# Performance work log

Hardware: AMD Instinct MI355X
Metric: run time of the kernel (lower is better)

The kernel has to match this reference:

```python
import jax, jax.numpy as jnp
import numpy as np

N = 50000
D = 128
E = 600000
R = 8


def setup_inputs() -> dict:
    key = jax.random.key(0)
    ks = jax.random.split(key, 8)
    x = jax.random.normal(ks[0], (N, D), dtype=jnp.float32)
    edge_index = jax.random.randint(ks[1], (2, E), 0, N, dtype=jnp.int64)
    edge_type = jax.random.randint(ks[2], (E,), 0, R, dtype=jnp.int64)
    scale = 1.0 / np.sqrt(D)
    w1 = jax.random.normal(ks[3], (R, D, D), dtype=jnp.float32) * scale
    root1 = jax.random.normal(ks[4], (D, D), dtype=jnp.float32) * scale
    b1 = jnp.zeros((D,), dtype=jnp.float32)
    w2 = jax.random.normal(ks[5], (R, D, D), dtype=jnp.float32) * scale
    root2 = jax.random.normal(ks[6], (D, D), dtype=jnp.float32) * scale
    b2 = jnp.zeros((D,), dtype=jnp.float32)
    return {"x": x, "edge_index": edge_index, "edge_type": edge_type,
            "w1": w1, "root1": root1, "b1": b1,
            "w2": w2, "root2": root2, "b2": b2}


def _rgcn_conv(x, edge_index, edge_type, w, root, b):
    # PyG RGCNConv: per-relation MEAN aggregation of source features over
    # incoming edges, then relation-specific linear, summed over relations,
    # plus root transform and bias.
    src, dst = edge_index[0], edge_index[1]
    # combined segment id: (dst_node, relation) -> one segment_sum pass
    seg = dst * R + edge_type  # [E]
    msgs = x[src]              # [E, D] gather
    sums = jax.ops.segment_sum(msgs, seg, num_segments=N * R).reshape(N, R, D)
    cnts = jax.ops.segment_sum(jnp.ones((msgs.shape[0],), dtype=x.dtype), seg,
                               num_segments=N * R).reshape(N, R, 1)
    mean = sums / jnp.maximum(cnts, 1.0)  # [N, R, D]; empty -> 0
    out = jnp.einsum('nrd,rde->ne', mean, w) + x @ root + b
    return out


def reference(x, edge_index, edge_type, w1, root1, b1, w2, root2, b2):
    # dropout is identity in eval mode
    h = jax.nn.relu(_rgcn_conv(x, edge_index, edge_type, w1, root1, b1))
    out = jax.nn.relu(_rgcn_conv(h, edge_index, edge_type, w2, root2, b2))
    return out
```

## Files before the change

kernel.cpp:

```cpp
#include <hip/hip_runtime.h>

#define NN 50000
#define D 128
#define EE 600000
#define R 8
#define NR (NN * R)
#define SCAN_CHUNK 1024
#define NSB ((NR + SCAN_CHUNK - 1) / SCAN_CHUNK)
#define KO 1152

typedef unsigned short u16;
typedef unsigned int u32;
typedef __attribute__((ext_vector_type(8))) short bf16x8;
typedef __attribute__((ext_vector_type(4))) float f32x4;

__device__ inline u16 f2bf(float f) {
    union { float f; u32 u; } v; v.f = f;
    return (u16)((v.u + 0x7FFFu + ((v.u >> 16) & 1u)) >> 16);
}
__device__ inline float bf2f(u16 h) {
    union { u32 u; float f; } v; v.u = ((u32)h) << 16;
    return v.f;
}

__global__ __launch_bounds__(256) void xcast_kernel(const float2* __restrict__ x2,
                                                    u32* __restrict__ xb, int n) {
    int i = blockIdx.x * 256 + threadIdx.x;
    if (i < n) {
        float2 v = x2[i];
        xb[i] = (u32)f2bf(v.x) | ((u32)f2bf(v.y) << 16);
    }
}

__global__ __launch_bounds__(256) void hist_kernel(const int* __restrict__ dst,
                                                   const int* __restrict__ et,
                                                   int* __restrict__ cnt, int E) {
    int e = blockIdx.x * 256 + threadIdx.x;
    if (e < E) atomicAdd(&cnt[dst[e] * R + et[e]], 1);
}

__global__ __launch_bounds__(256) void scanA(const int* __restrict__ cnt,
                                             int* __restrict__ off,
                                             int* __restrict__ bsum) {
    __shared__ int ts[256];
    const int b = blockIdx.x, t = threadIdx.x;
    const int base = b * SCAN_CHUNK + t * 4;
    int v0 = 0, v1 = 0, v2 = 0, v3 = 0;
    if (base + 3 < NR) {
        int4 q = *(const int4*)(cnt + base);
        v0 = q.x; v1 = q.y; v2 = q.z; v3 = q.w;
    } else {
        if (base < NR) v0 = cnt[base];
        if (base + 1 < NR) v1 = cnt[base + 1];
        if (base + 2 < NR) v2 = cnt[base + 2];
    }
    const int s = v0 + v1 + v2 + v3;
    ts[t] = s;
    __syncthreads();
    for (int d = 1; d < 256; d <<= 1) {
        int x = (t >= d) ? ts[t - d] : 0;
        __syncthreads();
        ts[t] += x;
        __syncthreads();
    }
    const int excl = ts[t] - s;
    if (base < NR) off[base] = excl;
    if (base + 1 < NR) off[base + 1] = excl + v0;
    if (base + 2 < NR) off[base + 2] = excl + v0 + v1;
    if (base + 3 < NR) off[base + 3] = excl + v0 + v1 + v2;
    if (t == 255) bsum[b] = ts[255];
}

__global__ __launch_bounds__(512) void scanB(const int* __restrict__ bsum,
                                             int* __restrict__ boff) {
    __shared__ int ts[512];
    const int t = threadIdx.x;
    const int v = (t < NSB) ? bsum[t] : 0;
    ts[t] = v;
    __syncthreads();
    for (int d = 1; d < 512; d <<= 1) {
        int x = (t >= d) ? ts[t - d] : 0;
        __syncthreads();
        ts[t] += x;
        __syncthreads();
    }
    if (t < NSB) boff[t] = ts[t] - v;
}

__global__ __launch_bounds__(256) void scanC(int* __restrict__ off,
                                             int* __restrict__ cursor,
                                             const int* __restrict__ boff) {
    const int b = blockIdx.x, t = threadIdx.x;
    const int add = boff[b];
    const int base = b * SCAN_CHUNK + t * 4;
#pragma unroll
    for (int j = 0; j < 4; ++j)
        if (base + j < NR) {
            int v = off[base + j] + add;
            off[base + j] = v;
            cursor[base + j] = v;
        }
    if (b == 0 && t == 0) off[NR] = EE;
}

__global__ __launch_bounds__(256) void place_kernel(const int* __restrict__ src,
                                                    const int* __restrict__ dst,
                                                    const int* __restrict__ et,
                                                    const int* __restrict__ cnt,
                                                    int* __restrict__ cursor,
                                                    uint2* __restrict__ edat, int E) {
    int e = blockIdx.x * 256 + threadIdx.x;
    if (e < E) {
        int r = et[e];
        int key = dst[e] * R + r;
        int p = atomicAdd(&cursor[key], 1);
        float s = 1.0f / (float)cnt[key];
        edat[p] = make_uint2((u32)src[e] * (KO / 2) + (u32)r * (D / 2),
                             __float_as_uint(s));
    }
}

__global__ __launch_bounds__(256) void bprep2_kernel(const float* __restrict__ w1,
                                                     const float* __restrict__ root1,
                                                     u16* __restrict__ Bf1,
                                                     const float* __restrict__ w2,
                                                     const float* __restrict__ root2,
                                                     u16* __restrict__ Bf2) {
    int gidx = blockIdx.x * 256 + threadIdx.x;
    if (gidx >= 2 * 9 * 4 * 8 * 64) return;
    const int layer = gidx / (9 * 4 * 8 * 64);
    const int idx = gidx - layer * (9 * 4 * 8 * 64);
    const float* w = layer ? w2 : w1;
    const float* root = layer ? root2 : root1;
    u16* Bfrag = layer ? Bf2 : Bf1;
    const int lane = idx & 63;
    const int g = (idx >> 6) & 7;
    const int kc = (idx >> 9) & 3;
    const int ct = idx >> 11;
    const int col = ct * 128 + g * 16 + (lane & 15);
    const int kbase = kc * 32 + (lane >> 4) * 8;
    u16* o = Bfrag + (size_t)idx * 8;
#pragma unroll
    for (int j = 0; j < 8; ++j) {
        const int k = kbase + j;
        float v = (col < R * D) ? w[(size_t)(col >> 7) * (D * D) + (size_t)k * D + (col & 127)]
                                : root[(size_t)k * D + (col - R * D)];
        o[j] = f2bf(v);
    }
}

__global__ __launch_bounds__(256, 4) void gemm_xw(const u16* __restrict__ xin,
                                                  const u16* __restrict__ Bfrag,
                                                  u16* __restrict__ y) {
    __shared__ uint4 Bs[2048];

    const int t = threadIdx.x;
    const int wave = t >> 6;
    const int lane = t & 63;
    const int quad = lane >> 4;
    const int l15 = lane & 15;
    const int n0 = blockIdx.x * 64;
    const int n = n0 + wave * 16 + l15;
    const int nc = (n < NN) ? n : (NN - 1);

    const u16* xr = xin + (size_t)nc * D + quad * 8;
    bf16x8 a0 = *(const bf16x8*)(xr);
    bf16x8 a1 = *(const bf16x8*)(xr + 32);
    bf16x8 a2 = *(const bf16x8*)(xr + 64);
    bf16x8 a3 = *(const bf16x8*)(xr + 96);

#pragma unroll 1
    for (int ct = 0; ct < 9; ++ct) {
        const uint4* bsrc = (const uint4*)Bfrag + (size_t)ct * 2048 + t;

        __syncthreads();
#pragma unroll
        for (int i = 0; i < 8; ++i) Bs[t + 256 * i] = bsrc[256 * i];
        __syncthreads();

        f32x4 acc[8];
#pragma unroll
        for (int g = 0; g < 8; ++g) acc[g] = (f32x4){0.f, 0.f, 0.f, 0.f};

        const u16* bb = (const u16*)Bs + lane * 8;
#pragma unroll
        for (int g = 0; g < 8; ++g) {
            bf16x8 b0 = *(const bf16x8*)(bb + (0 * 8 + g) * 512);
            acc[g] = __builtin_amdgcn_mfma_f32_16x16x32_bf16(a0, b0, acc[g], 0, 0, 0);
            bf16x8 b1 = *(const bf16x8*)(bb + (1 * 8 + g) * 512);
            acc[g] = __builtin_amdgcn_mfma_f32_16x16x32_bf16(a1, b1, acc[g], 0, 0, 0);
            bf16x8 b2 = *(const bf16x8*)(bb + (2 * 8 + g) * 512);
            acc[g] = __builtin_amdgcn_mfma_f32_16x16x32_bf16(a2, b2, acc[g], 0, 0, 0);
            bf16x8 b3 = *(const bf16x8*)(bb + (3 * 8 + g) * 512);
            acc[g] = __builtin_amdgcn_mfma_f32_16x16x32_bf16(a3, b3, acc[g], 0, 0, 0);
        }

#pragma unroll
        for (int g = 0; g < 8; ++g) {
            const int col = ct * 128 + g * 16 + l15;
#pragma unroll
            for (int q = 0; q < 4; ++q) {
                const int row = n0 + wave * 16 + quad * 4 + q;
                if (row < NN)
                    y[(size_t)row * KO + col] = f2bf(acc[g][q]);
            }
        }
    }
}

template <bool OUTBF>
__global__ __launch_bounds__(256) void agg_kernel(const u32* __restrict__ yv,
                                                  const int* __restrict__ off,
                                                  const uint2* __restrict__ edat,
                                                  const float* __restrict__ bias,
                                                  void* __restrict__ outp) {
    const int n = blockIdx.x * 4 + (threadIdx.x >> 6);
    const int lane = threadIdx.x & 63;
    const int e0 = off[n * 8], e1 = off[n * 8 + 8];

    float ax = 0.f, ay = 0.f;
    int cbase = e0;
    uint2 ev = make_uint2(0u, 0u);
    if (cbase + lane < e1) ev = edat[cbase + lane];

    int i = e0;
    while (i < e1) {
        const int chunk_end = (e1 < cbase + 64) ? e1 : (cbase + 64);
        for (; i + 3 < chunk_end; i += 4) {
            const int j = i - cbase;
            const u32 p0 = (u32)__shfl((int)ev.x, j);
            const u32 p1 = (u32)__shfl((int)ev.x, j + 1);
            const u32 p2 = (u32)__shfl((int)ev.x, j + 2);
            const u32 p3 = (u32)__shfl((int)ev.x, j + 3);
            const float f0 = __uint_as_float((u32)__shfl((int)ev.y, j));
            const float f1 = __uint_as_float((u32)__shfl((int)ev.y, j + 1));
            const float f2 = __uint_as_float((u32)__shfl((int)ev.y, j + 2));
            const float f3 = __uint_as_float((u32)__shfl((int)ev.y, j + 3));
            const u32 v0 = yv[(size_t)p0 + lane];
            const u32 v1 = yv[(size_t)p1 + lane];
            const u32 v2 = yv[(size_t)p2 + lane];
            const u32 v3 = yv[(size_t)p3 + lane];
            ax += f0 * bf2f((u16)(v0 & 0xFFFFu)); ay += f0 * bf2f((u16)(v0 >> 16));
            ax += f1 * bf2f((u16)(v1 & 0xFFFFu)); ay += f1 * bf2f((u16)(v1 >> 16));
            ax += f2 * bf2f((u16)(v2 & 0xFFFFu)); ay += f2 * bf2f((u16)(v2 >> 16));
            ax += f3 * bf2f((u16)(v3 & 0xFFFFu)); ay += f3 * bf2f((u16)(v3 >> 16));
        }
        for (; i < chunk_end; ++i) {
            const int j = i - cbase;
            const u32 p0 = (u32)__shfl((int)ev.x, j);
            const float f0 = __uint_as_float((u32)__shfl((int)ev.y, j));
            const u32 v0 = yv[(size_t)p0 + lane];
            ax += f0 * bf2f((u16)(v0 & 0xFFFFu));
            ay += f0 * bf2f((u16)(v0 >> 16));
        }
        if (i < e1) {
            cbase += 64;
            ev = (cbase + lane < e1) ? edat[cbase + lane] : make_uint2(0u, 0u);
        }
    }

    const u32 rv = yv[(size_t)n * (KO / 2) + (R * D / 2) + lane];
    const float2 bb = ((const float2*)bias)[lane];
    const float ox = fmaxf(ax + bf2f((u16)(rv & 0xFFFFu)) + bb.x, 0.f);
    const float oy = fmaxf(ay + bf2f((u16)(rv >> 16)) + bb.y, 0.f);
    if (OUTBF)
        ((u32*)outp)[(size_t)n * 64 + lane] = (u32)f2bf(ox) | ((u32)f2bf(oy) << 16);
    else
        ((float2*)outp)[(size_t)n * 64 + lane] = make_float2(ox, oy);
}

extern "C" void kernel_launch(void* const* d_in, const int* in_sizes, int n_in,
                              void* d_out, int out_size, void* d_ws, size_t ws_size,
                              hipStream_t stream) {
    const float* x = (const float*)d_in[0];
    const int* ei = (const int*)d_in[1];
    const int* et = (const int*)d_in[2];
    const float* w1 = (const float*)d_in[3];
    const float* root1 = (const float*)d_in[4];
    const float* b1 = (const float*)d_in[5];
    const float* w2 = (const float*)d_in[6];
    const float* root2 = (const float*)d_in[7];
    const float* b2 = (const float*)d_in[8];
    float* out = (float*)d_out;

    char* ws = (char*)d_ws;
    int* off    = (int*)(ws + 0);
    int* cnt_i  = (int*)(ws + 1600512);
    int* cursor = (int*)(ws + 3200512);
    int* bsum   = (int*)(ws + 4800512);
    int* boff   = (int*)(ws + 4802304);
    uint2* edat = (uint2*)(ws + 4804096);
    u32* xb     = (u32*)(ws + 9604096);
    u32* h      = (u32*)(ws + 22404096);
    u16* y      = (u16*)(ws + 35204096);
    u16* Bf1    = (u16*)(ws + 150404096);
    u16* Bf2    = (u16*)(ws + 150699008);

    const int* srcp = ei;
    const int* dstp = ei + EE;

    xcast_kernel<<<(NN * D / 2 + 255) / 256, 256, 0, stream>>>((const float2*)x,
                                                               xb, NN * D / 2);
    hipMemsetAsync(cnt_i, 0, (size_t)NR * sizeof(int), stream);
    hist_kernel<<<(EE + 255) / 256, 256, 0, stream>>>(dstp, et, cnt_i, EE);
    scanA<<<NSB, 256, 0, stream>>>(cnt_i, off, bsum);
    scanB<<<1, 512, 0, stream>>>(bsum, boff);
    scanC<<<NSB, 256, 0, stream>>>(off, cursor, boff);
    place_kernel<<<(EE + 255) / 256, 256, 0, stream>>>(srcp, dstp, et, cnt_i,
                                                       cursor, edat, EE);
    bprep2_kernel<<<(2 * 9 * 4 * 8 * 64 + 255) / 256, 256, 0, stream>>>(
        w1, root1, Bf1, w2, root2, Bf2);

    const int gemm_blocks = (NN + 63) / 64;
    const int agg_blocks = NN / 4;

    gemm_xw<<<gemm_blocks, 256, 0, stream>>>((const u16*)xb, Bf1, y);
    agg_kernel<true><<<agg_blocks, 256, 0, stream>>>((const u32*)y, off, edat,
                                                     b1, h);

    gemm_xw<<<gemm_blocks, 256, 0, stream>>>((const u16*)h, Bf2, y);
    agg_kernel<false><<<agg_blocks, 256, 0, stream>>>((const u32*)y, off, edat,
                                                      b2, out);
}
```

Baseline: 294.1 us.

## Fuse x cast into GEMM, merge scan passes, pack edge data to 32 bits

The separate fp32-to-bf16 cast kernel is removed, and the first GEMM now reads fp32 x and converts it in registers. scanB and scanC become a single kernel in which each block sums the preceding block totals itself. The count memset is folded into the weight-prep kernel. Edge records shrink from 8-byte (offset, scale) pairs to a 4-byte packed (src, relation), with the aggregation kernel recomputing the offset and the reciprocal count. The aim is fewer launches and less memory traffic, at the cost of a redundant prefix sum per block and an extra count load and division per edge chunk.

```diff
diff --git a/kernel.cpp b/kernel.cpp
--- a/kernel.cpp
+++ b/kernel.cpp
@@ -21,15 +21,6 @@
 __device__ inline float bf2f(u16 h) {
     union { u32 u; float f; } v; v.u = ((u32)h) << 16;
     return v.f;
-}
-
-__global__ __launch_bounds__(256) void xcast_kernel(const float2* __restrict__ x2,
-                                                    u32* __restrict__ xb, int n) {
-    int i = blockIdx.x * 256 + threadIdx.x;
-    if (i < n) {
-        float2 v = x2[i];
-        xb[i] = (u32)f2bf(v.x) | ((u32)f2bf(v.y) << 16);
-    }
 }
 
 __global__ __launch_bounds__(256) void hist_kernel(const int* __restrict__ dst,
@@ -71,27 +62,20 @@
     if (t == 255) bsum[b] = ts[255];
 }
 
-__global__ __launch_bounds__(512) void scanB(const int* __restrict__ bsum,
-                                             int* __restrict__ boff) {
-    __shared__ int ts[512];
-    const int t = threadIdx.x;
-    const int v = (t < NSB) ? bsum[t] : 0;
-    ts[t] = v;
+__global__ __launch_bounds__(256) void scanBC(int* __restrict__ off,
+                                              int* __restrict__ cursor,
+                                              const int* __restrict__ bsum) {
+    __shared__ int red[256];
+    const int b = blockIdx.x, t = threadIdx.x;
+    int p = 0;
+    for (int i = t; i < b; i += 256) p += bsum[i];
+    red[t] = p;
     __syncthreads();
-    for (int d = 1; d < 512; d <<= 1) {
-        int x = (t >= d) ? ts[t - d] : 0;
-        __syncthreads();
-        ts[t] += x;
-        __syncthreads();
-    }
-    if (t < NSB) boff[t] = ts[t] - v;
-}
-
-__global__ __launch_bounds__(256) void scanC(int* __restrict__ off,
-                                             int* __restrict__ cursor,
-                                             const int* __restrict__ boff) {
-    const int b = blockIdx.x, t = threadIdx.x;
-    const int add = boff[b];
+    for (int d = 128; d > 0; d >>= 1) {
+        if (t < d) red[t] += red[t + d];
+        __syncthreads();
+    }
+    const int add = red[0];
     const int base = b * SCAN_CHUNK + t * 4;
 #pragma unroll
     for (int j = 0; j < 4; ++j)
@@ -106,17 +90,14 @@
 __global__ __launch_bounds__(256) void place_kernel(const int* __restrict__ src,
                                                     const int* __restrict__ dst,
                                                     const int* __restrict__ et,
-                                                    const int* __restrict__ cnt,
                                                     int* __restrict__ cursor,
-                                                    uint2* __restrict__ edat, int E) {
+                                                    u32* __restrict__ epk, int E) {
     int e = blockIdx.x * 256 + threadIdx.x;
     if (e < E) {
         int r = et[e];
         int key = dst[e] * R + r;
         int p = atomicAdd(&cursor[key], 1);
-        float s = 1.0f / (float)cnt[key];
-        edat[p] = make_uint2((u32)src[e] * (KO / 2) + (u32)r * (D / 2),
-                             __float_as_uint(s));
+        epk[p] = ((u32)src[e] << 3) | (u32)r;
     }
 }
 
@@ -125,8 +106,11 @@
                                                      u16* __restrict__ Bf1,
                                                      const float* __restrict__ w2,
                                                      const float* __restrict__ root2,
-                                                     u16* __restrict__ Bf2) {
+                                                     u16* __restrict__ Bf2,
+                                                     int4* __restrict__ cntz) {
     int gidx = blockIdx.x * 256 + threadIdx.x;
+    for (int i = gidx; i < NR / 4; i += 36864)
+        cntz[i] = make_int4(0, 0, 0, 0);
     if (gidx >= 2 * 9 * 4 * 8 * 64) return;
     const int layer = gidx / (9 * 4 * 8 * 64);
     const int idx = gidx - layer * (9 * 4 * 8 * 64);
@@ -149,7 +133,8 @@
     }
 }
 
-__global__ __launch_bounds__(256, 4) void gemm_xw(const u16* __restrict__ xin,
+template <bool INF32>
+__global__ __launch_bounds__(256, 4) void gemm_xw(const void* __restrict__ xin,
                                                   const u16* __restrict__ Bfrag,
                                                   u16* __restrict__ y) {
     __shared__ uint4 Bs[2048];
@@ -163,11 +148,28 @@
     const int n = n0 + wave * 16 + l15;
     const int nc = (n < NN) ? n : (NN - 1);
 
-    const u16* xr = xin + (size_t)nc * D + quad * 8;
-    bf16x8 a0 = *(const bf16x8*)(xr);
-    bf16x8 a1 = *(const bf16x8*)(xr + 32);
-    bf16x8 a2 = *(const bf16x8*)(xr + 64);
-    bf16x8 a3 = *(const bf16x8*)(xr + 96);
+    bf16x8 a0, a1, a2, a3;
+    if (INF32) {
+        const float* xr = (const float*)xin + (size_t)nc * D + quad * 8;
+#pragma unroll
+        for (int c = 0; c < 4; ++c) {
+            float4 v0 = *(const float4*)(xr + c * 32);
+            float4 v1 = *(const float4*)(xr + c * 32 + 4);
+            bf16x8 a;
+            a[0] = (short)f2bf(v0.x); a[1] = (short)f2bf(v0.y);
+            a[2] = (short)f2bf(v0.z); a[3] = (short)f2bf(v0.w);
+            a[4] = (short)f2bf(v1.x); a[5] = (short)f2bf(v1.y);
+            a[6] = (short)f2bf(v1.z); a[7] = (short)f2bf(v1.w);
+            if (c == 0) a0 = a; else if (c == 1) a1 = a;
+            else if (c == 2) a2 = a; else a3 = a;
+        }
+    } else {
+        const u16* xr = (const u16*)xin + (size_t)nc * D + quad * 8;
+        a0 = *(const bf16x8*)(xr);
+        a1 = *(const bf16x8*)(xr + 32);
+        a2 = *(const bf16x8*)(xr + 64);
+        a3 = *(const bf16x8*)(xr + 96);
+    }
 
 #pragma unroll 1
     for (int ct = 0; ct < 9; ++ct) {
@@ -211,7 +213,8 @@
 template <bool OUTBF>
 __global__ __launch_bounds__(256) void agg_kernel(const u32* __restrict__ yv,
                                                   const int* __restrict__ off,
-                                                  const uint2* __restrict__ edat,
+                                                  const u32* __restrict__ epk,
+                                                  const int* __restrict__ cnt,
                                                   const float* __restrict__ bias,
                                                   void* __restrict__ outp) {
     const int n = blockIdx.x * 4 + (threadIdx.x >> 6);
@@ -220,22 +223,27 @@
 
     float ax = 0.f, ay = 0.f;
     int cbase = e0;
-    uint2 ev = make_uint2(0u, 0u);
-    if (cbase + lane < e1) ev = edat[cbase + lane];
+    u32 yoff = 0u; float sc = 0.f;
+    if (cbase + lane < e1) {
+        const u32 pk = epk[cbase + lane];
+        const int r = (int)(pk & 7u);
+        yoff = (pk >> 3) * (KO / 2) + (u32)r * (D / 2);
+        sc = 1.0f / (float)cnt[n * 8 + r];
+    }
 
     int i = e0;
     while (i < e1) {
         const int chunk_end = (e1 < cbase + 64) ? e1 : (cbase + 64);
         for (; i + 3 < chunk_end; i += 4) {
             const int j = i - cbase;
-            const u32 p0 = (u32)__shfl((int)ev.x, j);
-            const u32 p1 = (u32)__shfl((int)ev.x, j + 1);
-            const u32 p2 = (u32)__shfl((int)ev.x, j + 2);
-            const u32 p3 = (u32)__shfl((int)ev.x, j + 3);
-            const float f0 = __uint_as_float((u32)__shfl((int)ev.y, j));
-            const float f1 = __uint_as_float((u32)__shfl((int)ev.y, j + 1));
-            const float f2 = __uint_as_float((u32)__shfl((int)ev.y, j + 2));
-            const float f3 = __uint_as_float((u32)__shfl((int)ev.y, j + 3));
+            const u32 p0 = (u32)__shfl((int)yoff, j);
+            const u32 p1 = (u32)__shfl((int)yoff, j + 1);
+            const u32 p2 = (u32)__shfl((int)yoff, j + 2);
+            const u32 p3 = (u32)__shfl((int)yoff, j + 3);
+            const float f0 = __shfl(sc, j);
+            const float f1 = __shfl(sc, j + 1);
+            const float f2 = __shfl(sc, j + 2);
+            const float f3 = __shfl(sc, j + 3);
             const u32 v0 = yv[(size_t)p0 + lane];
             const u32 v1 = yv[(size_t)p1 + lane];
             const u32 v2 = yv[(size_t)p2 + lane];
@@ -247,15 +255,20 @@
         }
         for (; i < chunk_end; ++i) {
             const int j = i - cbase;
-            const u32 p0 = (u32)__shfl((int)ev.x, j);
-            const float f0 = __uint_as_float((u32)__shfl((int)ev.y, j));
+            const u32 p0 = (u32)__shfl((int)yoff, j);
+            const float f0 = __shfl(sc, j);
             const u32 v0 = yv[(size_t)p0 + lane];
             ax += f0 * bf2f((u16)(v0 & 0xFFFFu));
             ay += f0 * bf2f((u16)(v0 >> 16));
         }
         if (i < e1) {
             cbase += 64;
-            ev = (cbase + lane < e1) ? edat[cbase + lane] : make_uint2(0u, 0u);
+            if (cbase + lane < e1) {
+                const u32 pk = epk[cbase + lane];
+                const int r = (int)(pk & 7u);
+                yoff = (pk >> 3) * (KO / 2) + (u32)r * (D / 2);
+                sc = 1.0f / (float)cnt[n * 8 + r];
+            } else { yoff = 0u; sc = 0.f; }
         }
     }
 
@@ -288,37 +301,31 @@
     int* cnt_i  = (int*)(ws + 1600512);
     int* cursor = (int*)(ws + 3200512);
     int* bsum   = (int*)(ws + 4800512);
-    int* boff   = (int*)(ws + 4802304);
-    uint2* edat = (uint2*)(ws + 4804096);
-    u32* xb     = (u32*)(ws + 9604096);
-    u32* h      = (u32*)(ws + 22404096);
-    u16* y      = (u16*)(ws + 35204096);
-    u16* Bf1    = (u16*)(ws + 150404096);
-    u16* Bf2    = (u16*)(ws + 150699008);
+    u32* epk    = (u32*)(ws + 4804096);
+    u32* h      = (u32*)(ws + 7204096);
+    u16* y      = (u16*)(ws + 20004096);
+    u16* Bf1    = (u16*)(ws + 135204096);
+    u16* Bf2    = (u16*)(ws + 135499008);
 
     const int* srcp = ei;
     const int* dstp = ei + EE;
 
-    xcast_kernel<<<(NN * D / 2 + 255) / 256, 256, 0, stream>>>((const float2*)x,
-                                                               xb, NN * D / 2);
-    hipMemsetAsync(cnt_i, 0, (size_t)NR * sizeof(int), stream);
+    bprep2_kernel<<<144, 256, 0, stream>>>(w1, root1, Bf1, w2, root2, Bf2,
+                                           (int4*)cnt_i);
     hist_kernel<<<(EE + 255) / 256, 256, 0, stream>>>(dstp, et, cnt_i, EE);
     scanA<<<NSB, 256, 0, stream>>>(cnt_i, off, bsum);
-    scanB<<<1, 512, 0, stream>>>(bsum, boff);
-    scanC<<<NSB, 256, 0, stream>>>(off, cursor, boff);
-    place_kernel<<<(EE + 255) / 256, 256, 0, stream>>>(srcp, dstp, et, cnt_i,
-                                                       cursor, edat, EE);
-    bprep2_kernel<<<(2 * 9 * 4 * 8 * 64 + 255) / 256, 256, 0, stream>>>(
-        w1, root1, Bf1, w2, root2, Bf2);
+    scanBC<<<NSB, 256, 0, stream>>>(off, cursor, bsum);
+    place_kernel<<<(EE + 255) / 256, 256, 0, stream>>>(srcp, dstp, et, cursor,
+                                                       epk, EE);
 
     const int gemm_blocks = (NN + 63) / 64;
     const int agg_blocks = NN / 4;
 
-    gemm_xw<<<gemm_blocks, 256, 0, stream>>>((const u16*)xb, Bf1, y);
-    agg_kernel<true><<<agg_blocks, 256, 0, stream>>>((const u32*)y, off, edat,
-                                                     b1, h);
-
-    gemm_xw<<<gemm_blocks, 256, 0, stream>>>((const u16*)h, Bf2, y);
-    agg_kernel<false><<<agg_blocks, 256, 0, stream>>>((const u32*)y, off, edat,
-                                                      b2, out);
-}
+    gemm_xw<true><<<gemm_blocks, 256, 0, stream>>>(x, Bf1, y);
+    agg_kernel<true><<<agg_blocks, 256, 0, stream>>>((const u32*)y, off, epk,
+                                                     cnt_i, b1, h);
+
+    gemm_xw<false><<<gemm_blocks, 256, 0, stream>>>(h, Bf2, y);
+    agg_kernel<false><<<agg_blocks, 256, 0, stream>>>((const u32*)y, off, epk,
+                                                      cnt_i, b2, out);
+}
```

Result: faster. 284.2 us (-3.4%).
